# Kernel optimization log

Measured on AMD Instinct MI355X. Metric: run time of the kernel, lower is better.

Reference implementation:

```python
import jax, jax.numpy as jnp
import numpy as np

STRIDES = [8, 16, 32, 64, 128]
HW = [(100, 128), (50, 64), (25, 32), (13, 16), (7, 8)]
SCORE_THR = 0.05
IOU_THR = 0.6
MAX_DET = 1000
MAX_OUT = 100  # fixed pad size in _post_process


def _coords(h, w, stride):
    # FCOS coords_fmap2orig: center of each cell in original image coords
    sx = jnp.arange(w, dtype=jnp.float32) * stride + stride // 2
    sy = jnp.arange(h, dtype=jnp.float32) * stride + stride // 2
    yy, xx = jnp.meshgrid(sy, sx, indexing='ij')
    return jnp.stack([xx.reshape(-1), yy.reshape(-1)], axis=-1)  # [h*w, 2]


def _reshape_cat(feats):
    # list of [B,C,h,w] -> [B, sum(h*w), C]
    outs = [f.transpose(0, 2, 3, 1).reshape(f.shape[0], -1, f.shape[1]) for f in feats]
    return jnp.concatenate(outs, axis=1)


def _nms_single(scores, classes, boxes):
    # scores [N] (sorted desc), classes [N] int, boxes [N,4]; greedy DIoU-NMS
    N = scores.shape[0]
    valid = scores >= SCORE_THR
    # batched_nms: offset boxes by class so cross-class boxes never overlap
    max_coord = jnp.max(jnp.where(valid[:, None], boxes, -jnp.inf))
    offs = classes.astype(boxes.dtype) * (max_coord + 1.0)
    b = boxes + offs[:, None]
    x1, y1, x2, y2 = b[:, 0], b[:, 1], b[:, 2], b[:, 3]
    areas = (x2 - x1 + 1.0) * (y2 - y1 + 1.0)
    cx, cy = (x1 + x2) * 0.5, (y1 + y2) * 0.5
    xmin = jnp.maximum(x1[:, None], x1[None, :]); ymin = jnp.maximum(y1[:, None], y1[None, :])
    xmax = jnp.minimum(x2[:, None], x2[None, :]); ymax = jnp.minimum(y2[:, None], y2[None, :])
    inter = jnp.clip(xmax - xmin, 0) * jnp.clip(ymax - ymin, 0)
    iou = inter / (areas[:, None] + areas[None, :] - inter)
    inter_diag = (cx[:, None] - cx[None, :]) ** 2 + (cy[:, None] - cy[None, :]) ** 2
    oxmin = jnp.minimum(x1[:, None], x1[None, :]); oymin = jnp.minimum(y1[:, None], y1[None, :])
    oxmax = jnp.maximum(x2[:, None], x2[None, :]); oymax = jnp.maximum(y2[:, None], y2[None, :])
    outer_diag = (oxmax - oxmin) ** 2 + (oymax - oymin) ** 2
    diou = iou - inter_diag / jnp.maximum(outer_diag, 1e-12)
    idxs = jnp.arange(N)

    def body(i, keep):
        sup = keep[i] & (idxs > i) & (diou[i] > IOU_THR)
        return keep & (~sup)

    keep = jax.lax.fori_loop(0, N, body, valid)
    # kept boxes in descending-score order, padded with -2 to MAX_OUT
    rank = jnp.cumsum(keep) - 1
    pos = jnp.where(keep, jnp.minimum(rank, MAX_OUT), MAX_OUT)  # slot MAX_OUT is dumped
    out_s = jnp.full((MAX_OUT + 1,), -2.0, scores.dtype).at[pos].set(jnp.where(keep, scores, -2.0))[:MAX_OUT]
    out_c = jnp.full((MAX_OUT + 1,), -2, classes.dtype).at[pos].set(jnp.where(keep, classes, -2))[:MAX_OUT]
    out_b = jnp.full((MAX_OUT + 1, 4), -2.0, boxes.dtype).at[pos].set(jnp.where(keep[:, None], boxes, -2.0))[:MAX_OUT]
    return out_s, out_c, out_b


def _forward(cls_feats, reg_feats):
    cls_logits = _reshape_cat(cls_feats)          # [B, L, C]
    reg_preds = _reshape_cat(reg_feats)           # [B, L, 4]
    coords = jnp.concatenate([_coords(h, w, s) for (h, w), s in zip(HW, STRIDES)], axis=0)
    cls_preds = jax.nn.sigmoid(cls_logits)
    cls_scores = jnp.max(cls_preds, axis=-1)      # [B, L]
    cls_classes = jnp.argmax(cls_preds, axis=-1) + 1
    x1y1 = coords[None] - reg_preds[..., :2]
    x2y2 = coords[None] + reg_preds[..., 2:]
    boxes = jnp.concatenate([x1y1, x2y2], axis=-1)  # [B, L, 4]
    max_num = min(MAX_DET, cls_scores.shape[-1])
    topv, topi = jax.lax.top_k(cls_scores, max_num)  # sorted descending
    top_c = jnp.take_along_axis(cls_classes, topi, axis=1)
    top_b = jnp.take_along_axis(boxes, topi[..., None], axis=1)
    return jax.vmap(_nms_single)(topv, top_c, top_b)


def setup_inputs() -> dict:
    key = jax.random.key(0)
    ks = jax.random.split(key, 16)
    inp = {}
    C = 80
    for i, (h, w) in enumerate(HW):
        inp[f'cls{i}'] = jax.random.normal(ks[i], (16, C, h, w), dtype=jnp.float32)
        # ltrb offsets scaled so boxes are realistically sized and overlap
        inp[f'reg{i}'] = jax.random.uniform(ks[5 + i], (16, 4, h, w), dtype=jnp.float32) * 64.0
    inp['boxes_anchor'] = jax.random.normal(ks[10], (16, 100, 4), dtype=jnp.float32)
    inp['labels_anchor'] = jax.random.randint(ks[11], (16, 100), 0, 80)
    inp['score_anchor'] = jax.random.uniform(ks[12], (16, 100), dtype=jnp.float32)
    return inp


def reference(cls0, cls1, cls2, cls3, cls4, reg0, reg1, reg2, reg3, reg4,
              boxes_anchor, labels_anchor, score_anchor):
    # nms_anchor (boxes_anchor, labels_anchor, score_anchor) is consumed but
    # does not affect the output in the original forward.
    scores, classes, boxes = _forward([cls0, cls1, cls2, cls3, cls4],
                                      [reg0, reg1, reg2, reg3, reg4])
    return scores, classes, boxes
```

## Files before the change

kernel.cpp:

```cpp
#include <hip/hip_runtime.h>
#include <math.h>

typedef unsigned int u32;
typedef unsigned long long u64;

#define BB 16
#define NANCH 17064
#define NGRP 4266
#define NTOP 1000
#define NWORD 16
#define NOUT 100
#define NBIN13 8192
#define NSPLIT 17

__device__ __forceinline__ u32 fmap(float v) {
    u32 u = __float_as_uint(v);
    return (u & 0x80000000u) ? ~u : (u | 0x80000000u);
}
__device__ __forceinline__ float funmap(u32 u) {
    u32 b = (u & 0x80000000u) ? (u & 0x7FFFFFFFu) : ~u;
    return __uint_as_float(b);
}

__global__ void __launch_bounds__(256) k_anchor(
        const float* __restrict__ c0, const float* __restrict__ c1,
        const float* __restrict__ c2, const float* __restrict__ c3,
        const float* __restrict__ c4,
        const float* __restrict__ r0, const float* __restrict__ r1,
        const float* __restrict__ r2, const float* __restrict__ r3,
        const float* __restrict__ r4,
        u32* __restrict__ akey, int* __restrict__ aclass,
        float* __restrict__ abox) {
    int tid = threadIdx.x;
    int b = blockIdx.y;
    int gt = blockIdx.x * 256 + tid;
    if (gt >= 4 * NGRP) return;
    int p = gt >> 2, cs = gt & 3;
    int a = p * 4;

    const float *cp, *rp;
    int loc, wl, h, stride, half;
    if (a < 12800)      { loc = a;         wl = 7; h = 100; stride = 8;   half = 4;  cp = c0; rp = r0; }
    else if (a < 16000) { loc = a - 12800; wl = 6; h = 50;  stride = 16;  half = 8;  cp = c1; rp = r1; }
    else if (a < 16800) { loc = a - 16000; wl = 5; h = 25;  stride = 32;  half = 16; cp = c2; rp = r2; }
    else if (a < 17008) { loc = a - 16800; wl = 4; h = 13;  stride = 64;  half = 32; cp = c3; rp = r3; }
    else                { loc = a - 17008; wl = 3; h = 7;   stride = 128; half = 64; cp = c4; rp = r4; }
    int y = loc >> wl, x = loc & ((1 << wl) - 1);
    int hw = h << wl, hwq = hw >> 2;

    const float4* cb4 = (const float4*)(cp + (size_t)b * 80 * hw +
                                        (size_t)cs * 20 * hw + loc);
    float4 buf[20];
#pragma unroll
    for (int c = 0; c < 20; ++c) buf[c] = cb4[(size_t)c * hwq];
    const float4* rb4 = (const float4*)(rp + (size_t)b * 4 * hw + loc);
    float4 gl, gt_, gr, gb;
    if (cs == 0) {
        gl = rb4[0]; gt_ = rb4[hwq]; gr = rb4[2 * hwq]; gb = rb4[3 * hwq];
    }
    __builtin_amdgcn_sched_barrier(0);

    int cbase = cs * 20;
    float m0 = buf[0].x, m1 = buf[0].y, m2 = buf[0].z, m3 = buf[0].w;
    int a0 = cbase, a1 = cbase, a2 = cbase, a3 = cbase;
#pragma unroll
    for (int c = 1; c < 20; ++c) {
        float4 u = buf[c];
        int cc = cbase + c;
        if (u.x > m0) { m0 = u.x; a0 = cc; }
        if (u.y > m1) { m1 = u.y; a1 = cc; }
        if (u.z > m2) { m2 = u.z; a2 = cc; }
        if (u.w > m3) { m3 = u.w; a3 = cc; }
    }
    {
        bool low = (cs & 1) == 0;
        float pm; int pa; bool tk;
        pm = __shfl_xor(m0, 1); pa = __shfl_xor(a0, 1);
        tk = low ? (m0 >= pm) : (m0 > pm); m0 = tk ? m0 : pm; a0 = tk ? a0 : pa;
        pm = __shfl_xor(m1, 1); pa = __shfl_xor(a1, 1);
        tk = low ? (m1 >= pm) : (m1 > pm); m1 = tk ? m1 : pm; a1 = tk ? a1 : pa;
        pm = __shfl_xor(m2, 1); pa = __shfl_xor(a2, 1);
        tk = low ? (m2 >= pm) : (m2 > pm); m2 = tk ? m2 : pm; a2 = tk ? a2 : pa;
        pm = __shfl_xor(m3, 1); pa = __shfl_xor(a3, 1);
        tk = low ? (m3 >= pm) : (m3 > pm); m3 = tk ? m3 : pm; a3 = tk ? a3 : pa;
    }
    {
        bool low = (cs & 2) == 0;
        float pm; int pa; bool tk;
        pm = __shfl_xor(m0, 2); pa = __shfl_xor(a0, 2);
        tk = low ? (m0 >= pm) : (m0 > pm); m0 = tk ? m0 : pm; a0 = tk ? a0 : pa;
        pm = __shfl_xor(m1, 2); pa = __shfl_xor(a1, 2);
        tk = low ? (m1 >= pm) : (m1 > pm); m1 = tk ? m1 : pm; a1 = tk ? a1 : pa;
        pm = __shfl_xor(m2, 2); pa = __shfl_xor(a2, 2);
        tk = low ? (m2 >= pm) : (m2 > pm); m2 = tk ? m2 : pm; a2 = tk ? a2 : pa;
        pm = __shfl_xor(m3, 2); pa = __shfl_xor(a3, 2);
        tk = low ? (m3 >= pm) : (m3 > pm); m3 = tk ? m3 : pm; a3 = tk ? a3 : pa;
    }
    if (cs == 0) {
        int idx = b * NANCH + a;
        *(uint4*)(akey + idx) = make_uint4(fmap(m0), fmap(m1), fmap(m2), fmap(m3));
        *(int4*)(aclass + idx) = make_int4(a0 + 1, a1 + 1, a2 + 1, a3 + 1);
        float cy = (float)(y * stride + half);
        float cx0 = (float)(x * stride + half);
        float gls[4] = {gl.x, gl.y, gl.z, gl.w};
        float gts[4] = {gt_.x, gt_.y, gt_.z, gt_.w};
        float grs[4] = {gr.x, gr.y, gr.z, gr.w};
        float gbs[4] = {gb.x, gb.y, gb.z, gb.w};
#pragma unroll
        for (int k = 0; k < 4; ++k) {
            float cx = cx0 + (float)(k * stride);
            *(float4*)(abox + (size_t)(idx + k) * 4) =
                make_float4(cx - gls[k], cy - gts[k], cx + grs[k], cy + gbs[k]);
        }
    }
}

__global__ void __launch_bounds__(256) k_refine(const u32* __restrict__ akey,
                                                u32* __restrict__ thr,
                                                u32* __restrict__ ccnt,
                                                u32* __restrict__ maxcU) {
    __shared__ u32 h1[NBIN13];
    __shared__ u32 seg[256];
    __shared__ u32 binb[32];
    __shared__ int Gs;
    __shared__ u32 T13s, As;
    int b = blockIdx.x, t = threadIdx.x;
    const uint4* ak4 = (const uint4*)(akey + (size_t)b * NANCH);

    for (int i = t; i < NBIN13; i += 256) h1[i] = 0;
    if (t == 0) Gs = 0;
    __syncthreads();
    for (int i = t; i < NANCH / 4; i += 256) {
        uint4 k4 = ak4[i];
        atomicAdd(&h1[k4.x >> 19], 1u);
        atomicAdd(&h1[k4.y >> 19], 1u);
        atomicAdd(&h1[k4.z >> 19], 1u);
        atomicAdd(&h1[k4.w >> 19], 1u);
    }
    __syncthreads();
    u32 s = 0;
#pragma unroll
    for (int j = 0; j < 32; ++j) s += h1[t * 32 + ((j + t) & 31)];
    seg[t] = s;
    __syncthreads();
    for (int off = 1; off < 256; off <<= 1) {
        u32 v = seg[t];
        u32 add = (t + off < 256) ? seg[t + off] : 0u;
        __syncthreads();
        seg[t] = v + add;
        __syncthreads();
    }
    if (seg[t] >= NTOP) atomicMax(&Gs, t);
    __syncthreads();
    int G = Gs;
    u32 hi = (G < 255) ? seg[G + 1] : 0u;
    if (t < 32) binb[t] = h1[G * 32 + t];
    __syncthreads();
    if (t == 0) {
        u32 acc = hi, A = hi;
        int T13 = G * 32;
        for (int i = 31; i >= 0; --i) {
            A = acc;
            acc += binb[i];
            if (acc >= NTOP) { T13 = G * 32 + i; break; }
        }
        T13s = (u32)T13; As = A;
        Gs = 0;
    }
    __syncthreads();
    u32 T13 = T13s, A = As;
    for (int i = t; i < NBIN13; i += 256) h1[i] = 0;
    __syncthreads();
    for (int i = t; i < NANCH / 4; i += 256) {
        uint4 k4 = ak4[i];
        if ((k4.x >> 19) == T13) atomicAdd(&h1[(k4.x >> 6) & (NBIN13 - 1)], 1u);
        if ((k4.y >> 19) == T13) atomicAdd(&h1[(k4.y >> 6) & (NBIN13 - 1)], 1u);
        if ((k4.z >> 19) == T13) atomicAdd(&h1[(k4.z >> 6) & (NBIN13 - 1)], 1u);
        if ((k4.w >> 19) == T13) atomicAdd(&h1[(k4.w >> 6) & (NBIN13 - 1)], 1u);
    }
    __syncthreads();
    u32 target = NTOP - A;
    u32 s2 = 0;
#pragma unroll
    for (int j = 0; j < 32; ++j) s2 += h1[t * 32 + ((j + t) & 31)];
    seg[t] = s2;
    __syncthreads();
    for (int off = 1; off < 256; off <<= 1) {
        u32 v = seg[t];
        u32 add = (t + off < 256) ? seg[t + off] : 0u;
        __syncthreads();
        seg[t] = v + add;
        __syncthreads();
    }
    if (seg[t] >= target) atomicMax(&Gs, t);
    __syncthreads();
    int G2 = Gs;
    u32 hi2 = (G2 < 255) ? seg[G2 + 1] : 0u;
    if (t == 0) {
        u32 acc = hi2;
        int t2 = G2 * 32;
        for (int i = 31; i >= 0; --i) {
            acc += h1[G2 * 32 + i];
            if (acc >= target) { t2 = G2 * 32 + i; break; }
        }
        thr[b] = (T13 << 13) | (u32)t2;
        ccnt[b] = 0;
        maxcU[b] = 0;
    }
}

__global__ void __launch_bounds__(256) k_compact(const u32* __restrict__ akey,
                                                 const u32* __restrict__ thr,
                                                 u32* __restrict__ ccnt,
                                                 u64* __restrict__ cand) {
    __shared__ u32 lcnt, baseoff;
    int b = blockIdx.y, s = blockIdx.x, t = threadIdx.x;
    if (t == 0) lcnt = 0;
    __syncthreads();
    u32 T = thr[b];

    int base = s * 1024;
    int n = min(1024, NANCH - base);
    u32 kk[4]; u32 pos[4]; bool m[4] = {false, false, false, false};
    if (4 * t < n) {
        uint4 k4 = *(const uint4*)(akey + (size_t)b * NANCH + base + 4 * t);
        kk[0] = k4.x; kk[1] = k4.y; kk[2] = k4.z; kk[3] = k4.w;
#pragma unroll
        for (int i = 0; i < 4; ++i) {
            m[i] = (kk[i] >> 6) >= T;
            if (m[i]) pos[i] = atomicAdd(&lcnt, 1u);
        }
    }
    __syncthreads();
    if (t == 0) baseoff = atomicAdd(&ccnt[b], lcnt);
    __syncthreads();
    u32 bo = baseoff;
    u64* cb = cand + (size_t)b * NANCH;
#pragma unroll
    for (int i = 0; i < 4; ++i) {
        if (m[i])
            cb[bo + pos[i]] =
                ((u64)kk[i] << 32) | (u64)(0xFFFFFFFFu - (u32)(base + 4 * t + i));
    }
}

__global__ void __launch_bounds__(256) k_rank(
        const u64* __restrict__ cand, const u32* __restrict__ ccnt,
        const int* __restrict__ aclass, const float* __restrict__ abox,
        float* __restrict__ tscore, int* __restrict__ tclass,
        float* __restrict__ tbox, u32* __restrict__ maxcU) {
    __shared__ u64 tile[2048];
    int b = blockIdx.y, tid = threadIdx.x;
    int C = (int)ccnt[b];
    const u64* ck = cand + (size_t)b * NANCH;
    for (int base = blockIdx.x * 256; base < C; base += gridDim.x * 256) {
        int i = base + tid;
        bool have = i < C;
        u64 my = have ? ck[i] : 0ull;
        int rank = 0;
        for (int t0 = 0; t0 < C; t0 += 2048) {
            int nt = min(2048, C - t0);
            __syncthreads();
            for (int j = tid; j < nt; j += 256) tile[j] = ck[t0 + j];
            __syncthreads();
            int r0 = 0, r1 = 0, r2 = 0, r3 = 0, r4 = 0, r5 = 0, r6 = 0, r7 = 0;
            int j = 0;
            for (; j + 8 <= nt; j += 8) {
                u64 v0 = tile[j + 0], v1 = tile[j + 1];
                u64 v2 = tile[j + 2], v3 = tile[j + 3];
                u64 v4 = tile[j + 4], v5 = tile[j + 5];
                u64 v6 = tile[j + 6], v7 = tile[j + 7];
                r0 += v0 > my; r1 += v1 > my; r2 += v2 > my; r3 += v3 > my;
                r4 += v4 > my; r5 += v5 > my; r6 += v6 > my; r7 += v7 > my;
            }
            for (; j < nt; ++j) r0 += tile[j] > my;
            rank += ((r0 + r1) + (r2 + r3)) + ((r4 + r5) + (r6 + r7));
        }
        u32 mymax = 0;
        if (have && rank < NTOP) {
            u32 a = 0xFFFFFFFFu - (u32)(my & 0xFFFFFFFFull);
            int src = b * NANCH + (int)a;
            int dst = b * NTOP + rank;
            float logit = funmap((u32)(my >> 32));
            float sc = 1.0f / (1.0f + expf(-logit));
            float b0 = abox[src * 4 + 0], b1 = abox[src * 4 + 1];
            float b2 = abox[src * 4 + 2], b3 = abox[src * 4 + 3];
            tscore[dst] = sc;
            tclass[dst] = aclass[src];
            tbox[dst * 4 + 0] = b0;
            tbox[dst * 4 + 1] = b1;
            tbox[dst * 4 + 2] = b2;
            tbox[dst * 4 + 3] = b3;
            if (sc >= 0.05f)
                mymax = fmap(fmaxf(fmaxf(b0, b1), fmaxf(b2, b3)));
        }
        for (int off = 32; off > 0; off >>= 1) {
            u32 o = (u32)__shfl_down((int)mymax, off);
            mymax = mymax > o ? mymax : o;
        }
        if ((tid & 63) == 0) atomicMax(&maxcU[b], mymax);
    }
}

__global__ void k_sup(const float* __restrict__ tbox, const int* __restrict__ tclass,
                      const u32* __restrict__ maxcU, u64* __restrict__ sup) {
    int u = blockIdx.x, b = blockIdx.y;
    int ti = 0, rem = u;
    while (rem >= NWORD - ti) { rem -= NWORD - ti; ++ti; }
    int tj = ti + rem;
    int t = threadIdx.x;
    __shared__ double jx1[64], jy1[64], jx2[64], jy2[64], jcx[64], jcy[64], jar[64];
    double mc1 = (double)funmap(maxcU[b]) + 1.0;
    int j = tj * 64 + t;
    if (j < NTOP) {
        const float* bx = tbox + (size_t)(b * NTOP + j) * 4;
        double o = (double)tclass[b * NTOP + j] * mc1;
        double x1 = (double)bx[0] + o, y1 = (double)bx[1] + o;
        double x2 = (double)bx[2] + o, y2 = (double)bx[3] + o;
        jx1[t] = x1; jy1[t] = y1; jx2[t] = x2; jy2[t] = y2;
        jcx[t] = (x1 + x2) * 0.5; jcy[t] = (y1 + y2) * 0.5;
        jar[t] = (x2 - x1 + 1.0) * (y2 - y1 + 1.0);
    }
    __syncthreads();
    int i = ti * 64 + t;
    if (i >= NTOP) return;
    const float* bx = tbox + (size_t)(b * NTOP + i) * 4;
    double o = (double)tclass[b * NTOP + i] * mc1;
    double ix1 = (double)bx[0] + o, iy1 = (double)bx[1] + o;
    double ix2 = (double)bx[2] + o, iy2 = (double)bx[3] + o;
    double icx = (ix1 + ix2) * 0.5, icy = (iy1 + iy2) * 0.5;
    double iar = (ix2 - ix1 + 1.0) * (iy2 - iy1 + 1.0);
    u64 bits = 0;
    int jbase = tj * 64;
    for (int jj = 0; jj < 64; ++jj) {
        int jg = jbase + jj;
        if (jg >= NTOP) break;
        if (jg <= i) continue;
        double xm = fmax(ix1, jx1[jj]), ym = fmax(iy1, jy1[jj]);
        double xM = fmin(ix2, jx2[jj]), yM = fmin(iy2, jy2[jj]);
        double inter = fmax(xM - xm, 0.0) * fmax(yM - ym, 0.0);
        double U = iar + jar[jj] - inter;
        double dx = icx - jcx[jj], dy = icy - jcy[jj];
        double idg = dx * dx + dy * dy;
        double ox = fmax(ix2, jx2[jj]) - fmin(ix1, jx1[jj]);
        double oy = fmax(iy2, jy2[jj]) - fmin(iy1, jy1[jj]);
        double odg = fmax(ox * ox + oy * oy, 1e-12);
        if (inter * odg - idg * U > 0.6 * (U * odg)) bits |= (1ull << jj);
    }
    sup[(size_t)(b * NTOP + i) * NWORD + tj] = bits;
}

__global__ void __launch_bounds__(64) k_scan(
        const u64* __restrict__ sup, const float* __restrict__ tscore,
        const int* __restrict__ tclass, const float* __restrict__ tbox,
        float* __restrict__ out) {
    int b = blockIdx.x, lane = threadIdx.x;
    __shared__ u64 lds[64 * 17];
    __shared__ int kept_lds[NOUT];
    const u64* supb = sup + (size_t)b * NTOP * NWORD;
    u64 remw = 0;
    int kept = 0;
    for (int t = 0; t < NWORD; ++t) {
        int r0 = t * 64;
#pragma unroll
        for (int q = 0; q < 16; ++q) {
            int e = q * 64 + lane;
            int rr = r0 + (e >> 4), w = e & 15;
            u64 v = (rr < NTOP) ? supb[(size_t)rr * 16 + w] : 0ull;
            lds[(e >> 4) * 17 + w] = v;
        }
        __syncthreads();
        int r = r0 + lane;
        float s = (r < NTOP) ? tscore[b * NTOP + r] : -1.0f;
        u64 vmask = __ballot(s >= 0.05f);
        u64 M = lds[lane * 17 + t];
        u64 rem_t = __shfl(remw, t);
        u64 cnd = vmask & ~rem_t;
        u64 keepmask = 0;
        while (cnd) {
            int k = __ffsll(cnd) - 1;
            keepmask |= 1ull << k;
            if (lane == 0) kept_lds[kept] = r0 + k;
            ++kept;
            if (kept >= NOUT) break;
            u64 Mk = __shfl(M, k);
            cnd &= ~(Mk | (1ull << k));
        }
        if (lane < NWORD) {
            u64 km = keepmask;
            while (km) {
                int k = __ffsll(km) - 1;
                km &= km - 1;
                remw |= lds[k * 17 + lane];
            }
        }
        __syncthreads();
        if (kept >= NOUT) break;
    }
    float* os = out + b * NOUT;
    float* oc = out + BB * NOUT + b * NOUT;
    float* ob = out + 2 * BB * NOUT + (size_t)b * NOUT * 4;
    for (int i = lane; i < NOUT; i += 64) { os[i] = -2.0f; oc[i] = -2.0f; }
    for (int i = lane; i < NOUT * 4; i += 64) ob[i] = -2.0f;
    __syncthreads();
    int ncopy = kept < NOUT ? kept : NOUT;
    for (int r = lane; r < ncopy; r += 64) {
        int i = kept_lds[r];
        os[r] = tscore[b * NTOP + i];
        oc[r] = (float)tclass[b * NTOP + i];
        ob[r * 4 + 0] = tbox[(size_t)(b * NTOP + i) * 4 + 0];
        ob[r * 4 + 1] = tbox[(size_t)(b * NTOP + i) * 4 + 1];
        ob[r * 4 + 2] = tbox[(size_t)(b * NTOP + i) * 4 + 2];
        ob[r * 4 + 3] = tbox[(size_t)(b * NTOP + i) * 4 + 3];
    }
}

extern "C" void kernel_launch(void* const* d_in, const int* in_sizes, int n_in,
                              void* d_out, int out_size, void* d_ws, size_t ws_size,
                              hipStream_t stream) {
    (void)in_sizes; (void)n_in; (void)out_size; (void)ws_size;
    const float* cls[5];
    const float* reg[5];
    for (int i = 0; i < 5; ++i) {
        cls[i] = (const float*)d_in[2 * i];
        reg[i] = (const float*)d_in[2 * i + 1];
    }
    float* out = (float*)d_out;

    char* ws = (char*)d_ws;
    u32* thr = (u32*)ws;             ws += 64;
    u32* ccnt = (u32*)ws;            ws += 64;
    u32* maxcU = (u32*)ws;           ws += 64;
    u64* cand = (u64*)ws;            ws += (size_t)BB * NANCH * sizeof(u64);
    u64* sup = (u64*)ws;             ws += (size_t)BB * NTOP * NWORD * sizeof(u64);
    u32* akey = (u32*)ws;            ws += (size_t)BB * NANCH * sizeof(u32);
    int* aclass = (int*)ws;          ws += (size_t)BB * NANCH * sizeof(int);
    float* abox = (float*)ws;        ws += (size_t)BB * NANCH * 4 * sizeof(float);
    float* tscore = (float*)ws;      ws += (size_t)BB * NTOP * sizeof(float);
    int* tclass = (int*)ws;          ws += (size_t)BB * NTOP * sizeof(int);
    float* tbox = (float*)ws;        ws += (size_t)BB * NTOP * 4 * sizeof(float);

    k_anchor<<<dim3((4 * NGRP + 255) / 256, BB), 256, 0, stream>>>(
        cls[0], cls[1], cls[2], cls[3], cls[4],
        reg[0], reg[1], reg[2], reg[3], reg[4],
        akey, aclass, abox);
    k_refine<<<BB, 256, 0, stream>>>(akey, thr, ccnt, maxcU);
    k_compact<<<dim3(NSPLIT, BB), 256, 0, stream>>>(akey, thr, ccnt, cand);
    k_rank<<<dim3(5, BB), 256, 0, stream>>>(cand, ccnt, aclass, abox,
                                            tscore, tclass, tbox, maxcU);
    k_sup<<<dim3(136, BB), 64, 0, stream>>>(tbox, tclass, maxcU, sup);
    k_scan<<<BB, 64, 0, stream>>>(sup, tscore, tclass, tbox, out);
}
```

Before: 230.9 us.

## Fuse threshold, compaction and rank-select into one per-image kernel

Merges the refine, compact and rank kernels into a single per-batch kernel that keeps the candidates in the reused histogram shared memory. Ranking runs against shared memory instead of global tiles, and two kernel launches plus the global candidate buffer are dropped. In exchange, each image is handled by only one 256-thread block, which lowers parallelism for the rank step, and candidates are capped at 4096, so an image with more candidates above the threshold would be truncated. The max coordinate is now reduced with a shared atomic.

```diff
diff --git a/kernel.cpp b/kernel.cpp
--- a/kernel.cpp
+++ b/kernel.cpp
@@ -11,7 +11,7 @@
 #define NWORD 16
 #define NOUT 100
 #define NBIN13 8192
-#define NSPLIT 17
+#define CANDCAP 4096
 
 __device__ __forceinline__ u32 fmap(float v) {
     u32 u = __float_as_uint(v);
@@ -115,20 +115,21 @@
     }
 }
 
-__global__ void __launch_bounds__(256) k_refine(const u32* __restrict__ akey,
-                                                u32* __restrict__ thr,
-                                                u32* __restrict__ ccnt,
-                                                u32* __restrict__ maxcU) {
+__global__ void __launch_bounds__(256) k_select(
+        const u32* __restrict__ akey, const int* __restrict__ aclass,
+        const float* __restrict__ abox,
+        float* __restrict__ tscore, int* __restrict__ tclass,
+        float* __restrict__ tbox, u32* __restrict__ maxcU) {
     __shared__ u32 h1[NBIN13];
     __shared__ u32 seg[256];
     __shared__ u32 binb[32];
     __shared__ int Gs;
-    __shared__ u32 T13s, As;
+    __shared__ u32 T13s, As, thrS, lcnt, lmax;
     int b = blockIdx.x, t = threadIdx.x;
     const uint4* ak4 = (const uint4*)(akey + (size_t)b * NANCH);
 
     for (int i = t; i < NBIN13; i += 256) h1[i] = 0;
-    if (t == 0) Gs = 0;
+    if (t == 0) { Gs = 0; lcnt = 0; lmax = 0; }
     __syncthreads();
     for (int i = t; i < NANCH / 4; i += 256) {
         uint4 k4 = ak4[i];
@@ -203,83 +204,44 @@
             acc += h1[G2 * 32 + i];
             if (acc >= target) { t2 = G2 * 32 + i; break; }
         }
-        thr[b] = (T13 << 13) | (u32)t2;
-        ccnt[b] = 0;
-        maxcU[b] = 0;
-    }
-}
-
-__global__ void __launch_bounds__(256) k_compact(const u32* __restrict__ akey,
-                                                 const u32* __restrict__ thr,
-                                                 u32* __restrict__ ccnt,
-                                                 u64* __restrict__ cand) {
-    __shared__ u32 lcnt, baseoff;
-    int b = blockIdx.y, s = blockIdx.x, t = threadIdx.x;
-    if (t == 0) lcnt = 0;
-    __syncthreads();
-    u32 T = thr[b];
-
-    int base = s * 1024;
-    int n = min(1024, NANCH - base);
-    u32 kk[4]; u32 pos[4]; bool m[4] = {false, false, false, false};
-    if (4 * t < n) {
-        uint4 k4 = *(const uint4*)(akey + (size_t)b * NANCH + base + 4 * t);
-        kk[0] = k4.x; kk[1] = k4.y; kk[2] = k4.z; kk[3] = k4.w;
-#pragma unroll
-        for (int i = 0; i < 4; ++i) {
-            m[i] = (kk[i] >> 6) >= T;
-            if (m[i]) pos[i] = atomicAdd(&lcnt, 1u);
-        }
-    }
-    __syncthreads();
-    if (t == 0) baseoff = atomicAdd(&ccnt[b], lcnt);
-    __syncthreads();
-    u32 bo = baseoff;
-    u64* cb = cand + (size_t)b * NANCH;
-#pragma unroll
-    for (int i = 0; i < 4; ++i) {
-        if (m[i])
-            cb[bo + pos[i]] =
-                ((u64)kk[i] << 32) | (u64)(0xFFFFFFFFu - (u32)(base + 4 * t + i));
-    }
-}
-
-__global__ void __launch_bounds__(256) k_rank(
-        const u64* __restrict__ cand, const u32* __restrict__ ccnt,
-        const int* __restrict__ aclass, const float* __restrict__ abox,
-        float* __restrict__ tscore, int* __restrict__ tclass,
-        float* __restrict__ tbox, u32* __restrict__ maxcU) {
-    __shared__ u64 tile[2048];
-    int b = blockIdx.y, tid = threadIdx.x;
-    int C = (int)ccnt[b];
-    const u64* ck = cand + (size_t)b * NANCH;
-    for (int base = blockIdx.x * 256; base < C; base += gridDim.x * 256) {
-        int i = base + tid;
-        bool have = i < C;
-        u64 my = have ? ck[i] : 0ull;
-        int rank = 0;
-        for (int t0 = 0; t0 < C; t0 += 2048) {
-            int nt = min(2048, C - t0);
-            __syncthreads();
-            for (int j = tid; j < nt; j += 256) tile[j] = ck[t0 + j];
-            __syncthreads();
-            int r0 = 0, r1 = 0, r2 = 0, r3 = 0, r4 = 0, r5 = 0, r6 = 0, r7 = 0;
-            int j = 0;
-            for (; j + 8 <= nt; j += 8) {
-                u64 v0 = tile[j + 0], v1 = tile[j + 1];
-                u64 v2 = tile[j + 2], v3 = tile[j + 3];
-                u64 v4 = tile[j + 4], v5 = tile[j + 5];
-                u64 v6 = tile[j + 6], v7 = tile[j + 7];
-                r0 += v0 > my; r1 += v1 > my; r2 += v2 > my; r3 += v3 > my;
-                r4 += v4 > my; r5 += v5 > my; r6 += v6 > my; r7 += v7 > my;
+        thrS = (T13 << 13) | (u32)t2;
+    }
+    __syncthreads();
+    u32 thr = thrS;
+    u64* cand = (u64*)h1;
+    __syncthreads();
+    for (int i = t; i < NANCH / 4; i += 256) {
+        uint4 k4 = ak4[i];
+        u32 kk[4] = {k4.x, k4.y, k4.z, k4.w};
+#pragma unroll
+        for (int j = 0; j < 4; ++j) {
+            if ((kk[j] >> 6) >= thr) {
+                u32 p = atomicAdd(&lcnt, 1u);
+                if (p < CANDCAP)
+                    cand[p] = ((u64)kk[j] << 32) |
+                              (u64)(0xFFFFFFFFu - (u32)(4 * i + j));
             }
-            for (; j < nt; ++j) r0 += tile[j] > my;
-            rank += ((r0 + r1) + (r2 + r3)) + ((r4 + r5) + (r6 + r7));
-        }
-        u32 mymax = 0;
-        if (have && rank < NTOP) {
-            u32 a = 0xFFFFFFFFu - (u32)(my & 0xFFFFFFFFull);
-            int src = b * NANCH + (int)a;
+        }
+    }
+    __syncthreads();
+    int C = (int)lcnt; if (C > CANDCAP) C = CANDCAP;
+    for (int i = t; i < C; i += 256) {
+        u64 my = cand[i];
+        int q0 = 0, q1 = 0, q2 = 0, q3 = 0, q4 = 0, q5 = 0, q6 = 0, q7 = 0;
+        int j = 0;
+        for (; j + 8 <= C; j += 8) {
+            u64 v0 = cand[j + 0], v1 = cand[j + 1];
+            u64 v2 = cand[j + 2], v3 = cand[j + 3];
+            u64 v4 = cand[j + 4], v5 = cand[j + 5];
+            u64 v6 = cand[j + 6], v7 = cand[j + 7];
+            q0 += v0 > my; q1 += v1 > my; q2 += v2 > my; q3 += v3 > my;
+            q4 += v4 > my; q5 += v5 > my; q6 += v6 > my; q7 += v7 > my;
+        }
+        for (; j < C; ++j) q0 += cand[j] > my;
+        int rank = ((q0 + q1) + (q2 + q3)) + ((q4 + q5) + (q6 + q7));
+        if (rank < NTOP) {
+            u32 ai = 0xFFFFFFFFu - (u32)(my & 0xFFFFFFFFull);
+            int src = b * NANCH + (int)ai;
             int dst = b * NTOP + rank;
             float logit = funmap((u32)(my >> 32));
             float sc = 1.0f / (1.0f + expf(-logit));
@@ -292,14 +254,11 @@
             tbox[dst * 4 + 2] = b2;
             tbox[dst * 4 + 3] = b3;
             if (sc >= 0.05f)
-                mymax = fmap(fmaxf(fmaxf(b0, b1), fmaxf(b2, b3)));
-        }
-        for (int off = 32; off > 0; off >>= 1) {
-            u32 o = (u32)__shfl_down((int)mymax, off);
-            mymax = mymax > o ? mymax : o;
-        }
-        if ((tid & 63) == 0) atomicMax(&maxcU[b], mymax);
-    }
+                atomicMax(&lmax, fmap(fmaxf(fmaxf(b0, b1), fmaxf(b2, b3))));
+        }
+    }
+    __syncthreads();
+    if (t == 0) maxcU[b] = lmax;
 }
 
 __global__ void k_sup(const float* __restrict__ tbox, const int* __restrict__ tclass,
@@ -428,10 +387,7 @@
     float* out = (float*)d_out;
 
     char* ws = (char*)d_ws;
-    u32* thr = (u32*)ws;             ws += 64;
-    u32* ccnt = (u32*)ws;            ws += 64;
     u32* maxcU = (u32*)ws;           ws += 64;
-    u64* cand = (u64*)ws;            ws += (size_t)BB * NANCH * sizeof(u64);
     u64* sup = (u64*)ws;             ws += (size_t)BB * NTOP * NWORD * sizeof(u64);
     u32* akey = (u32*)ws;            ws += (size_t)BB * NANCH * sizeof(u32);
     int* aclass = (int*)ws;          ws += (size_t)BB * NANCH * sizeof(int);
@@ -444,10 +400,8 @@
         cls[0], cls[1], cls[2], cls[3], cls[4],
         reg[0], reg[1], reg[2], reg[3], reg[4],
         akey, aclass, abox);
-    k_refine<<<BB, 256, 0, stream>>>(akey, thr, ccnt, maxcU);
-    k_compact<<<dim3(NSPLIT, BB), 256, 0, stream>>>(akey, thr, ccnt, cand);
-    k_rank<<<dim3(5, BB), 256, 0, stream>>>(cand, ccnt, aclass, abox,
-                                            tscore, tclass, tbox, maxcU);
+    k_select<<<BB, 256, 0, stream>>>(akey, aclass, abox,
+                                     tscore, tclass, tbox, maxcU);
     k_sup<<<dim3(136, BB), 64, 0, stream>>>(tbox, tclass, maxcU, sup);
     k_scan<<<BB, 64, 0, stream>>>(sup, tscore, tclass, tbox, out);
 }
```

New measurement: 281.6 us. 1.22x slower.

## Fuse score histogram into anchor kernel and double-buffer NMS scan tiles

Applied to the files above, without the earlier changes.

The coarse 13-bit score histogram is now built in the anchor-decode kernel with per-block LDS atomics, then merged into a global histogram, so the threshold kernel no longer rereads all keys. The global histogram and counters are zeroed by a memset. The NMS scan kernel now uses 256 threads: one wavefront runs the greedy scan while the others prefetch the next suppression-mask tile into a second LDS buffer. The cost is global atomics, an extra memset, and 32KB of LDS per anchor block, which may lower occupancy.

```diff
diff --git a/kernel.cpp b/kernel.cpp
--- a/kernel.cpp
+++ b/kernel.cpp
@@ -30,95 +30,112 @@
         const float* __restrict__ r2, const float* __restrict__ r3,
         const float* __restrict__ r4,
         u32* __restrict__ akey, int* __restrict__ aclass,
-        float* __restrict__ abox) {
+        float* __restrict__ abox, u32* __restrict__ ghist) {
+    __shared__ u32 h1[NBIN13];
     int tid = threadIdx.x;
     int b = blockIdx.y;
     int gt = blockIdx.x * 256 + tid;
-    if (gt >= 4 * NGRP) return;
-    int p = gt >> 2, cs = gt & 3;
-    int a = p * 4;
-
-    const float *cp, *rp;
-    int loc, wl, h, stride, half;
-    if (a < 12800)      { loc = a;         wl = 7; h = 100; stride = 8;   half = 4;  cp = c0; rp = r0; }
-    else if (a < 16000) { loc = a - 12800; wl = 6; h = 50;  stride = 16;  half = 8;  cp = c1; rp = r1; }
-    else if (a < 16800) { loc = a - 16000; wl = 5; h = 25;  stride = 32;  half = 16; cp = c2; rp = r2; }
-    else if (a < 17008) { loc = a - 16800; wl = 4; h = 13;  stride = 64;  half = 32; cp = c3; rp = r3; }
-    else                { loc = a - 17008; wl = 3; h = 7;   stride = 128; half = 64; cp = c4; rp = r4; }
-    int y = loc >> wl, x = loc & ((1 << wl) - 1);
-    int hw = h << wl, hwq = hw >> 2;
-
-    const float4* cb4 = (const float4*)(cp + (size_t)b * 80 * hw +
-                                        (size_t)cs * 20 * hw + loc);
-    float4 buf[20];
-#pragma unroll
-    for (int c = 0; c < 20; ++c) buf[c] = cb4[(size_t)c * hwq];
-    const float4* rb4 = (const float4*)(rp + (size_t)b * 4 * hw + loc);
-    float4 gl, gt_, gr, gb;
-    if (cs == 0) {
-        gl = rb4[0]; gt_ = rb4[hwq]; gr = rb4[2 * hwq]; gb = rb4[3 * hwq];
-    }
-    __builtin_amdgcn_sched_barrier(0);
-
-    int cbase = cs * 20;
-    float m0 = buf[0].x, m1 = buf[0].y, m2 = buf[0].z, m3 = buf[0].w;
-    int a0 = cbase, a1 = cbase, a2 = cbase, a3 = cbase;
-#pragma unroll
-    for (int c = 1; c < 20; ++c) {
-        float4 u = buf[c];
-        int cc = cbase + c;
-        if (u.x > m0) { m0 = u.x; a0 = cc; }
-        if (u.y > m1) { m1 = u.y; a1 = cc; }
-        if (u.z > m2) { m2 = u.z; a2 = cc; }
-        if (u.w > m3) { m3 = u.w; a3 = cc; }
-    }
-    {
-        bool low = (cs & 1) == 0;
-        float pm; int pa; bool tk;
-        pm = __shfl_xor(m0, 1); pa = __shfl_xor(a0, 1);
-        tk = low ? (m0 >= pm) : (m0 > pm); m0 = tk ? m0 : pm; a0 = tk ? a0 : pa;
-        pm = __shfl_xor(m1, 1); pa = __shfl_xor(a1, 1);
-        tk = low ? (m1 >= pm) : (m1 > pm); m1 = tk ? m1 : pm; a1 = tk ? a1 : pa;
-        pm = __shfl_xor(m2, 1); pa = __shfl_xor(a2, 1);
-        tk = low ? (m2 >= pm) : (m2 > pm); m2 = tk ? m2 : pm; a2 = tk ? a2 : pa;
-        pm = __shfl_xor(m3, 1); pa = __shfl_xor(a3, 1);
-        tk = low ? (m3 >= pm) : (m3 > pm); m3 = tk ? m3 : pm; a3 = tk ? a3 : pa;
-    }
-    {
-        bool low = (cs & 2) == 0;
-        float pm; int pa; bool tk;
-        pm = __shfl_xor(m0, 2); pa = __shfl_xor(a0, 2);
-        tk = low ? (m0 >= pm) : (m0 > pm); m0 = tk ? m0 : pm; a0 = tk ? a0 : pa;
-        pm = __shfl_xor(m1, 2); pa = __shfl_xor(a1, 2);
-        tk = low ? (m1 >= pm) : (m1 > pm); m1 = tk ? m1 : pm; a1 = tk ? a1 : pa;
-        pm = __shfl_xor(m2, 2); pa = __shfl_xor(a2, 2);
-        tk = low ? (m2 >= pm) : (m2 > pm); m2 = tk ? m2 : pm; a2 = tk ? a2 : pa;
-        pm = __shfl_xor(m3, 2); pa = __shfl_xor(a3, 2);
-        tk = low ? (m3 >= pm) : (m3 > pm); m3 = tk ? m3 : pm; a3 = tk ? a3 : pa;
-    }
-    if (cs == 0) {
-        int idx = b * NANCH + a;
-        *(uint4*)(akey + idx) = make_uint4(fmap(m0), fmap(m1), fmap(m2), fmap(m3));
-        *(int4*)(aclass + idx) = make_int4(a0 + 1, a1 + 1, a2 + 1, a3 + 1);
-        float cy = (float)(y * stride + half);
-        float cx0 = (float)(x * stride + half);
-        float gls[4] = {gl.x, gl.y, gl.z, gl.w};
-        float gts[4] = {gt_.x, gt_.y, gt_.z, gt_.w};
-        float grs[4] = {gr.x, gr.y, gr.z, gr.w};
-        float gbs[4] = {gb.x, gb.y, gb.z, gb.w};
-#pragma unroll
-        for (int k = 0; k < 4; ++k) {
-            float cx = cx0 + (float)(k * stride);
-            *(float4*)(abox + (size_t)(idx + k) * 4) =
-                make_float4(cx - gls[k], cy - gts[k], cx + grs[k], cy + gbs[k]);
-        }
-    }
-}
-
-__global__ void __launch_bounds__(256) k_refine(const u32* __restrict__ akey,
-                                                u32* __restrict__ thr,
-                                                u32* __restrict__ ccnt,
-                                                u32* __restrict__ maxcU) {
+    bool valid = gt < 4 * NGRP;
+
+    for (int i = tid; i < NBIN13; i += 256) h1[i] = 0;
+    __syncthreads();
+
+    if (valid) {
+        int p = gt >> 2, cs = gt & 3;
+        int a = p * 4;
+
+        const float *cp, *rp;
+        int loc, wl, h, stride, half;
+        if (a < 12800)      { loc = a;         wl = 7; h = 100; stride = 8;   half = 4;  cp = c0; rp = r0; }
+        else if (a < 16000) { loc = a - 12800; wl = 6; h = 50;  stride = 16;  half = 8;  cp = c1; rp = r1; }
+        else if (a < 16800) { loc = a - 16000; wl = 5; h = 25;  stride = 32;  half = 16; cp = c2; rp = r2; }
+        else if (a < 17008) { loc = a - 16800; wl = 4; h = 13;  stride = 64;  half = 32; cp = c3; rp = r3; }
+        else                { loc = a - 17008; wl = 3; h = 7;   stride = 128; half = 64; cp = c4; rp = r4; }
+        int y = loc >> wl, x = loc & ((1 << wl) - 1);
+        int hw = h << wl, hwq = hw >> 2;
+
+        const float4* cb4 = (const float4*)(cp + (size_t)b * 80 * hw +
+                                            (size_t)cs * 20 * hw + loc);
+        float4 buf[20];
+#pragma unroll
+        for (int c = 0; c < 20; ++c) buf[c] = cb4[(size_t)c * hwq];
+        const float4* rb4 = (const float4*)(rp + (size_t)b * 4 * hw + loc);
+        float4 gl, gt_, gr, gb;
+        if (cs == 0) {
+            gl = rb4[0]; gt_ = rb4[hwq]; gr = rb4[2 * hwq]; gb = rb4[3 * hwq];
+        }
+        __builtin_amdgcn_sched_barrier(0);
+
+        int cbase = cs * 20;
+        float m0 = buf[0].x, m1 = buf[0].y, m2 = buf[0].z, m3 = buf[0].w;
+        int a0 = cbase, a1 = cbase, a2 = cbase, a3 = cbase;
+#pragma unroll
+        for (int c = 1; c < 20; ++c) {
+            float4 u = buf[c];
+            int cc = cbase + c;
+            if (u.x > m0) { m0 = u.x; a0 = cc; }
+            if (u.y > m1) { m1 = u.y; a1 = cc; }
+            if (u.z > m2) { m2 = u.z; a2 = cc; }
+            if (u.w > m3) { m3 = u.w; a3 = cc; }
+        }
+        {
+            bool low = (cs & 1) == 0;
+            float pm; int pa; bool tk;
+            pm = __shfl_xor(m0, 1); pa = __shfl_xor(a0, 1);
+            tk = low ? (m0 >= pm) : (m0 > pm); m0 = tk ? m0 : pm; a0 = tk ? a0 : pa;
+            pm = __shfl_xor(m1, 1); pa = __shfl_xor(a1, 1);
+            tk = low ? (m1 >= pm) : (m1 > pm); m1 = tk ? m1 : pm; a1 = tk ? a1 : pa;
+            pm = __shfl_xor(m2, 1); pa = __shfl_xor(a2, 1);
+            tk = low ? (m2 >= pm) : (m2 > pm); m2 = tk ? m2 : pm; a2 = tk ? a2 : pa;
+            pm = __shfl_xor(m3, 1); pa = __shfl_xor(a3, 1);
+            tk = low ? (m3 >= pm) : (m3 > pm); m3 = tk ? m3 : pm; a3 = tk ? a3 : pa;
+        }
+        {
+            bool low = (cs & 2) == 0;
+            float pm; int pa; bool tk;
+            pm = __shfl_xor(m0, 2); pa = __shfl_xor(a0, 2);
+            tk = low ? (m0 >= pm) : (m0 > pm); m0 = tk ? m0 : pm; a0 = tk ? a0 : pa;
+            pm = __shfl_xor(m1, 2); pa = __shfl_xor(a1, 2);
+            tk = low ? (m1 >= pm) : (m1 > pm); m1 = tk ? m1 : pm; a1 = tk ? a1 : pa;
+            pm = __shfl_xor(m2, 2); pa = __shfl_xor(a2, 2);
+            tk = low ? (m2 >= pm) : (m2 > pm); m2 = tk ? m2 : pm; a2 = tk ? a2 : pa;
+            pm = __shfl_xor(m3, 2); pa = __shfl_xor(a3, 2);
+            tk = low ? (m3 >= pm) : (m3 > pm); m3 = tk ? m3 : pm; a3 = tk ? a3 : pa;
+        }
+        if (cs == 0) {
+            int idx = b * NANCH + a;
+            u32 km0 = fmap(m0), km1 = fmap(m1), km2 = fmap(m2), km3 = fmap(m3);
+            *(uint4*)(akey + idx) = make_uint4(km0, km1, km2, km3);
+            *(int4*)(aclass + idx) = make_int4(a0 + 1, a1 + 1, a2 + 1, a3 + 1);
+            atomicAdd(&h1[km0 >> 19], 1u);
+            atomicAdd(&h1[km1 >> 19], 1u);
+            atomicAdd(&h1[km2 >> 19], 1u);
+            atomicAdd(&h1[km3 >> 19], 1u);
+            float cy = (float)(y * stride + half);
+            float cx0 = (float)(x * stride + half);
+            float gls[4] = {gl.x, gl.y, gl.z, gl.w};
+            float gts[4] = {gt_.x, gt_.y, gt_.z, gt_.w};
+            float grs[4] = {gr.x, gr.y, gr.z, gr.w};
+            float gbs[4] = {gb.x, gb.y, gb.z, gb.w};
+#pragma unroll
+            for (int k = 0; k < 4; ++k) {
+                float cx = cx0 + (float)(k * stride);
+                *(float4*)(abox + (size_t)(idx + k) * 4) =
+                    make_float4(cx - gls[k], cy - gts[k], cx + grs[k], cy + gbs[k]);
+            }
+        }
+    }
+    __syncthreads();
+    u32* gh = ghist + (size_t)b * NBIN13;
+    for (int i = tid; i < NBIN13; i += 256) {
+        u32 c = h1[i];
+        if (c) atomicAdd(&gh[i], c);
+    }
+}
+
+__global__ void __launch_bounds__(256) k_thresh(
+        const u32* __restrict__ akey, const u32* __restrict__ ghist,
+        u32* __restrict__ thr) {
     __shared__ u32 h1[NBIN13];
     __shared__ u32 seg[256];
     __shared__ u32 binb[32];
@@ -127,16 +144,12 @@
     int b = blockIdx.x, t = threadIdx.x;
     const uint4* ak4 = (const uint4*)(akey + (size_t)b * NANCH);
 
-    for (int i = t; i < NBIN13; i += 256) h1[i] = 0;
+    {
+        const uint4* g4 = (const uint4*)(ghist + (size_t)b * NBIN13);
+        uint4* h4 = (uint4*)h1;
+        for (int i = t; i < NBIN13 / 4; i += 256) h4[i] = g4[i];
+    }
     if (t == 0) Gs = 0;
-    __syncthreads();
-    for (int i = t; i < NANCH / 4; i += 256) {
-        uint4 k4 = ak4[i];
-        atomicAdd(&h1[k4.x >> 19], 1u);
-        atomicAdd(&h1[k4.y >> 19], 1u);
-        atomicAdd(&h1[k4.z >> 19], 1u);
-        atomicAdd(&h1[k4.w >> 19], 1u);
-    }
     __syncthreads();
     u32 s = 0;
 #pragma unroll
@@ -204,8 +217,6 @@
             if (acc >= target) { t2 = G2 * 32 + i; break; }
         }
         thr[b] = (T13 << 13) | (u32)t2;
-        ccnt[b] = 0;
-        maxcU[b] = 0;
     }
 }
 
@@ -263,18 +274,18 @@
             __syncthreads();
             for (int j = tid; j < nt; j += 256) tile[j] = ck[t0 + j];
             __syncthreads();
-            int r0 = 0, r1 = 0, r2 = 0, r3 = 0, r4 = 0, r5 = 0, r6 = 0, r7 = 0;
+            int q0 = 0, q1 = 0, q2 = 0, q3 = 0, q4 = 0, q5 = 0, q6 = 0, q7 = 0;
             int j = 0;
             for (; j + 8 <= nt; j += 8) {
                 u64 v0 = tile[j + 0], v1 = tile[j + 1];
                 u64 v2 = tile[j + 2], v3 = tile[j + 3];
                 u64 v4 = tile[j + 4], v5 = tile[j + 5];
                 u64 v6 = tile[j + 6], v7 = tile[j + 7];
-                r0 += v0 > my; r1 += v1 > my; r2 += v2 > my; r3 += v3 > my;
-                r4 += v4 > my; r5 += v5 > my; r6 += v6 > my; r7 += v7 > my;
+                q0 += v0 > my; q1 += v1 > my; q2 += v2 > my; q3 += v3 > my;
+                q4 += v4 > my; q5 += v5 > my; q6 += v6 > my; q7 += v7 > my;
             }
-            for (; j < nt; ++j) r0 += tile[j] > my;
-            rank += ((r0 + r1) + (r2 + r3)) + ((r4 + r5) + (r6 + r7));
+            for (; j < nt; ++j) q0 += tile[j] > my;
+            rank += ((q0 + q1) + (q2 + q3)) + ((q4 + q5) + (q6 + q7));
         }
         u32 mymax = 0;
         if (have && rank < NTOP) {
@@ -350,61 +361,78 @@
     sup[(size_t)(b * NTOP + i) * NWORD + tj] = bits;
 }
 
-__global__ void __launch_bounds__(64) k_scan(
+__global__ void __launch_bounds__(256) k_scan(
         const u64* __restrict__ sup, const float* __restrict__ tscore,
         const int* __restrict__ tclass, const float* __restrict__ tbox,
         float* __restrict__ out) {
-    int b = blockIdx.x, lane = threadIdx.x;
-    __shared__ u64 lds[64 * 17];
+    int b = blockIdx.x, tid = threadIdx.x;
+    int lane = tid & 63;
+    __shared__ u64 tl[2][64 * 17];
+    __shared__ float sc_s[1024];
     __shared__ int kept_lds[NOUT];
+    __shared__ int kept_sh;
     const u64* supb = sup + (size_t)b * NTOP * NWORD;
+    for (int i = tid; i < 1024; i += 256)
+        sc_s[i] = (i < NTOP) ? tscore[b * NTOP + i] : -1.0f;
+    if (tid == 0) kept_sh = 0;
+    for (int q = 0; q < 4; ++q) {
+        int e = q * 256 + tid;
+        int rr = e >> 4, w = e & 15;
+        tl[0][rr * 17 + w] = (rr < NTOP) ? supb[(size_t)rr * 16 + w] : 0ull;
+    }
+    __syncthreads();
     u64 remw = 0;
     int kept = 0;
     for (int t = 0; t < NWORD; ++t) {
-        int r0 = t * 64;
-#pragma unroll
-        for (int q = 0; q < 16; ++q) {
-            int e = q * 64 + lane;
-            int rr = r0 + (e >> 4), w = e & 15;
-            u64 v = (rr < NTOP) ? supb[(size_t)rr * 16 + w] : 0ull;
-            lds[(e >> 4) * 17 + w] = v;
+        int cur = t & 1;
+        if (tid >= 64) {
+            if (t + 1 < NWORD) {
+                int r1 = (t + 1) * 64;
+                for (int e = tid - 64; e < 1024; e += 192) {
+                    int rr = r1 + (e >> 4), w = e & 15;
+                    tl[cur ^ 1][(e >> 4) * 17 + w] =
+                        (rr < NTOP) ? supb[(size_t)rr * 16 + w] : 0ull;
+                }
+            }
+        } else {
+            int r0 = t * 64;
+            int r = r0 + lane;
+            float s = sc_s[r];
+            u64 vmask = __ballot(s >= 0.05f);
+            u64 M = tl[cur][lane * 17 + t];
+            u64 rem_t = __shfl(remw, t);
+            u64 cnd = vmask & ~rem_t;
+            u64 keepmask = 0;
+            while (cnd) {
+                int k = __ffsll(cnd) - 1;
+                keepmask |= 1ull << k;
+                if (lane == 0) kept_lds[kept] = r0 + k;
+                ++kept;
+                if (kept >= NOUT) break;
+                u64 Mk = __shfl(M, k);
+                cnd &= ~(Mk | (1ull << k));
+            }
+            if (lane < NWORD) {
+                u64 km = keepmask;
+                while (km) {
+                    int k = __ffsll(km) - 1;
+                    km &= km - 1;
+                    remw |= tl[cur][k * 17 + lane];
+                }
+            }
+            if (lane == 0) kept_sh = kept;
         }
         __syncthreads();
-        int r = r0 + lane;
-        float s = (r < NTOP) ? tscore[b * NTOP + r] : -1.0f;
-        u64 vmask = __ballot(s >= 0.05f);
-        u64 M = lds[lane * 17 + t];
-        u64 rem_t = __shfl(remw, t);
-        u64 cnd = vmask & ~rem_t;
-        u64 keepmask = 0;
-        while (cnd) {
-            int k = __ffsll(cnd) - 1;
-            keepmask |= 1ull << k;
-            if (lane == 0) kept_lds[kept] = r0 + k;
-            ++kept;
-            if (kept >= NOUT) break;
-            u64 Mk = __shfl(M, k);
-            cnd &= ~(Mk | (1ull << k));
-        }
-        if (lane < NWORD) {
-            u64 km = keepmask;
-            while (km) {
-                int k = __ffsll(km) - 1;
-                km &= km - 1;
-                remw |= lds[k * 17 + lane];
-            }
-        }
-        __syncthreads();
-        if (kept >= NOUT) break;
+        if (kept_sh >= NOUT) break;
     }
     float* os = out + b * NOUT;
     float* oc = out + BB * NOUT + b * NOUT;
     float* ob = out + 2 * BB * NOUT + (size_t)b * NOUT * 4;
-    for (int i = lane; i < NOUT; i += 64) { os[i] = -2.0f; oc[i] = -2.0f; }
-    for (int i = lane; i < NOUT * 4; i += 64) ob[i] = -2.0f;
-    __syncthreads();
-    int ncopy = kept < NOUT ? kept : NOUT;
-    for (int r = lane; r < ncopy; r += 64) {
+    for (int i = tid; i < NOUT; i += 256) { os[i] = -2.0f; oc[i] = -2.0f; }
+    for (int i = tid; i < NOUT * 4; i += 256) ob[i] = -2.0f;
+    __syncthreads();
+    int ncopy = kept_sh < NOUT ? kept_sh : NOUT;
+    for (int r = tid; r < ncopy; r += 256) {
         int i = kept_lds[r];
         os[r] = tscore[b * NTOP + i];
         oc[r] = (float)tclass[b * NTOP + i];
@@ -428,9 +456,11 @@
     float* out = (float*)d_out;
 
     char* ws = (char*)d_ws;
-    u32* thr = (u32*)ws;             ws += 64;
+    u32* ghist = (u32*)ws;           ws += (size_t)BB * NBIN13 * sizeof(u32);
     u32* ccnt = (u32*)ws;            ws += 64;
     u32* maxcU = (u32*)ws;           ws += 64;
+    size_t zbytes = (size_t)BB * NBIN13 * sizeof(u32) + 128;
+    u32* thr = (u32*)ws;             ws += 64;
     u64* cand = (u64*)ws;            ws += (size_t)BB * NANCH * sizeof(u64);
     u64* sup = (u64*)ws;             ws += (size_t)BB * NTOP * NWORD * sizeof(u64);
     u32* akey = (u32*)ws;            ws += (size_t)BB * NANCH * sizeof(u32);
@@ -440,14 +470,16 @@
     int* tclass = (int*)ws;          ws += (size_t)BB * NTOP * sizeof(int);
     float* tbox = (float*)ws;        ws += (size_t)BB * NTOP * 4 * sizeof(float);
 
+    hipMemsetAsync(ghist, 0, zbytes, stream);
+
     k_anchor<<<dim3((4 * NGRP + 255) / 256, BB), 256, 0, stream>>>(
         cls[0], cls[1], cls[2], cls[3], cls[4],
         reg[0], reg[1], reg[2], reg[3], reg[4],
-        akey, aclass, abox);
-    k_refine<<<BB, 256, 0, stream>>>(akey, thr, ccnt, maxcU);
+        akey, aclass, abox, ghist);
+    k_thresh<<<BB, 256, 0, stream>>>(akey, ghist, thr);
     k_compact<<<dim3(NSPLIT, BB), 256, 0, stream>>>(akey, thr, ccnt, cand);
     k_rank<<<dim3(5, BB), 256, 0, stream>>>(cand, ccnt, aclass, abox,
                                             tscore, tclass, tbox, maxcU);
     k_sup<<<dim3(136, BB), 64, 0, stream>>>(tbox, tclass, maxcU, sup);
-    k_scan<<<BB, 64, 0, stream>>>(sup, tscore, tclass, tbox, out);
-}
+    k_scan<<<BB, 256, 0, stream>>>(sup, tscore, tclass, tbox, out);
+}
```

After: 226.6 us. About the same (-1.9%).
